# Optimization experiments

Measured on AMD Instinct MI355X. Metric: run time of the kernel, lower is better.

Reference implementation:

```python
import jax, jax.numpy as jnp
import numpy as np

N_HEAD = 16
HEAD_DIM = 64

def setup_inputs() -> dict:
    key = jax.random.key(0)
    k1, k2, k3 = jax.random.split(key, 3)
    B, S, D = 4, 2048, 1024
    x = jax.random.normal(k1, (B, S, D), dtype=jnp.float32)
    mask = jnp.tril(jnp.ones((S, S), dtype=bool))[None, None]  # (1,1,S,S) causal
    w_attn = jax.random.normal(k2, (D, 3 * D), dtype=jnp.float32) * (1.0 / np.sqrt(D))
    b_attn = jnp.zeros((3 * D,), dtype=jnp.float32)
    w_proj = jax.random.normal(k3, (D, D), dtype=jnp.float32) * (1.0 / np.sqrt(D))
    b_proj = jnp.zeros((D,), dtype=jnp.float32)
    return {"x": x, "mask": mask, "w_attn": w_attn, "b_attn": b_attn,
            "w_proj": w_proj, "b_proj": b_proj}

def reference(x, mask, w_attn, b_attn, w_proj, b_proj):
    B, S, D = x.shape
    H, hd = N_HEAD, HEAD_DIM
    qkv = x @ w_attn + b_attn                      # (B,S,3D)
    q, k, v = jnp.split(qkv, 3, axis=-1)
    q = q.reshape(B, S, H, hd).transpose(0, 2, 1, 3)  # (B,H,S,hd)
    k = k.reshape(B, S, H, hd).transpose(0, 2, 1, 3)
    v = v.reshape(B, S, H, hd).transpose(0, 2, 1, 3)
    scores = jnp.einsum('bhqd,bhkd->bhqk', q, k) / jnp.sqrt(jnp.float32(hd))
    scores = jnp.where(mask, scores, jnp.float32(-1e10))
    weights = jax.nn.softmax(scores, axis=-1)      # dropout is identity (deterministic=True)
    attn = jnp.einsum('bhqk,bhkd->bhqd', weights, v)
    attn = attn.transpose(0, 2, 1, 3).reshape(B, S, D)
    return attn @ w_proj + b_proj
```

## Files before the change

### kernel.cpp

```cpp
#include <hip/hip_runtime.h>
#include <hip/hip_bf16.h>
#include <stdint.h>


typedef uint16_t u16;
typedef __bf16 bf16x8 __attribute__((ext_vector_type(8)));
typedef __bf16 bf16x4 __attribute__((ext_vector_type(4)));
typedef short s16x4 __attribute__((ext_vector_type(4)));
typedef float f32x4 __attribute__((ext_vector_type(4)));

#define S_LEN 2048
#define DMODEL 1024
#define NHEAD 16
#define HDIM 64
#define MTOT 8192
#define NQKV 3072

__device__ __forceinline__ u16 f2bf(float f) {
    union { float f; uint32_t u; } v; v.f = f;
    uint32_t u = v.u;
    return (u16)((u + 0x7fffu + ((u >> 16) & 1u)) >> 16);
}

__device__ __forceinline__ s16x4 bits4(bf16x4 v) {
    union { bf16x4 b; s16x4 s; } u; u.b = v; return u.s;
}

__device__ __forceinline__ f32x4 mfma16(bf16x4 a, bf16x4 b, f32x4 c) {
    return __builtin_amdgcn_mfma_f32_16x16x16bf16_1k(bits4(a), bits4(b), c, 0, 0, 0);
}

__device__ __forceinline__ void async_load16(const void* g, void* l) {
    __builtin_amdgcn_global_load_lds(
        (__attribute__((address_space(1))) void*)g,
        (__attribute__((address_space(3))) void*)l,
        16, 0, 0);
}

__global__ void convert_x_kernel(const float4* __restrict__ in, ushort4* __restrict__ out, int n4) {
    int i = blockIdx.x * 256 + threadIdx.x;
    if (i < n4) {
        float4 f = in[i];
        ushort4 o;
        o.x = f2bf(f.x); o.y = f2bf(f.y); o.z = f2bf(f.z); o.w = f2bf(f.w);
        out[i] = o;
    }
}

__global__ void transpose_bf16_kernel(const float* __restrict__ in, u16* __restrict__ out, int R, int C) {
    __shared__ float tile[64][65];
    int r0 = blockIdx.y * 64, c0 = blockIdx.x * 64;
    #pragma unroll
    for (int i = 0; i < 16; ++i) {
        int idx = threadIdx.x + i * 256;
        int r = idx >> 6, c = idx & 63;
        tile[r][c] = in[(size_t)(r0 + r) * C + c0 + c];
    }
    __syncthreads();
    #pragma unroll
    for (int i = 0; i < 16; ++i) {
        int idx = threadIdx.x + i * 256;
        int c = idx >> 6, r = idx & 63;
        out[(size_t)(c0 + c) * R + r0 + r] = f2bf(tile[r][c]);
    }
}

__global__ void transpose_v_kernel(const u16* __restrict__ qkv, u16* __restrict__ vt) {
    __shared__ u16 tile[64 * 66];
    const int tid = threadIdx.x;
    const int stile = blockIdx.x, bh = blockIdx.y;
    const int b = bh >> 4, h = bh & 15;
    const u16* src = qkv + ((size_t)b * S_LEN + stile * 64) * NQKV + 2 * DMODEL + h * HDIM;
    #pragma unroll
    for (int it = 0; it < 2; ++it) {
        int item = it * 256 + tid;
        int s = item >> 3, d0 = (item & 7) * 8;
        bf16x8 v = *(const bf16x8*)(src + (size_t)s * NQKV + d0);
        const u16* vu = (const u16*)&v;
        #pragma unroll
        for (int j = 0; j < 8; ++j) tile[(d0 + j) * 66 + s] = vu[j];
    }
    __syncthreads();
    #pragma unroll
    for (int it = 0; it < 2; ++it) {
        int item = it * 256 + tid;
        int d = item >> 3, s0 = (item & 7) * 8;
        union { u16 u[8]; uint4 v; } pk;
        #pragma unroll
        for (int j = 0; j < 8; ++j) pk.u[j] = tile[d * 66 + s0 + j];
        *(uint4*)(vt + ((size_t)bh * 64 + d) * S_LEN + stile * 64 + s0) = pk.v;
    }
}

template<bool OUT_BF16>
__global__ __launch_bounds__(256, 3) void gemm_bt(
    const u16* __restrict__ A, const u16* __restrict__ Bt,
    const float* __restrict__ bias, void* __restrict__ C,
    int M, int N, int K)
{
    __shared__ __attribute__((aligned(16))) u16 As[128 * 32];
    __shared__ __attribute__((aligned(16))) u16 Bs[128 * 32];
    const int tid = threadIdx.x;
    const int wave = tid >> 6, lane = tid & 63;
    const int l15 = lane & 15, q4 = lane >> 4;
    const int wm = wave >> 1, wn = wave & 1;

    const int gx = gridDim.x, gy = gridDim.y;
    int bid = (int)blockIdx.y * gx + (int)blockIdx.x;
    const int PANEL = 8;
    int panel = bid / (PANEL * gy);
    int within = bid - panel * (PANEL * gy);
    int mb = panel * PANEL + (within % PANEL);
    int nb = within / PANEL;
    const int m0 = mb * 128, n0 = nb * 128;

    f32x4 acc[4][4] = {};

    const int srow = lane >> 2;
    const int scol = (lane & 3) * 8;

    for (int k0 = 0; k0 < K; k0 += 32) {
        #pragma unroll
        for (int q = 0; q < 2; ++q) {
            int r = wave * 32 + q * 16 + srow;
            async_load16(A  + (size_t)(m0 + r) * K + k0 + scol, As + (wave * 32 + q * 16) * 32);
            async_load16(Bt + (size_t)(n0 + r) * K + k0 + scol, Bs + (wave * 32 + q * 16) * 32);
        }
        __syncthreads();

        bf16x8 af[4], bfr[4];
        #pragma unroll
        for (int t = 0; t < 4; ++t) {
            af[t]  = *(const bf16x8*)(As + (wm * 64 + t * 16 + l15) * 32 + q4 * 8);
            bfr[t] = *(const bf16x8*)(Bs + (wn * 64 + t * 16 + l15) * 32 + q4 * 8);
        }
        #pragma unroll
        for (int tm = 0; tm < 4; ++tm)
            #pragma unroll
            for (int tn = 0; tn < 4; ++tn)
                acc[tm][tn] = __builtin_amdgcn_mfma_f32_16x16x32_bf16(af[tm], bfr[tn], acc[tm][tn], 0, 0, 0);
        __syncthreads();
    }

    #pragma unroll
    for (int tm = 0; tm < 4; ++tm) {
        int row = m0 + wm * 64 + tm * 16 + q4 * 4;
        #pragma unroll
        for (int tn = 0; tn < 4; ++tn) {
            int col = n0 + wn * 64 + tn * 16 + l15;
            float bv = bias[col];
            #pragma unroll
            for (int r2 = 0; r2 < 4; ++r2) {
                float v = acc[tm][tn][r2] + bv;
                if (OUT_BF16) ((u16*)C)[(size_t)(row + r2) * N + col] = f2bf(v);
                else          ((float*)C)[(size_t)(row + r2) * N + col] = v;
            }
        }
    }
}

__device__ __forceinline__ void stage_tiles(
    const u16* __restrict__ qkv, const u16* __restrict__ vt,
    size_t base, int bh, int h, int w, int srow8, int schunk,
    int kt, u16* __restrict__ KsB, u16* __restrict__ VsB)
{
    #pragma unroll
    for (int q = 0; q < 2; ++q) {
        int rloc = w * 16 + q * 8 + srow8;
        int sc = ((schunk ^ (rloc & 7)) * 8);
        async_load16(qkv + (base + (size_t)kt * 64 + rloc) * (size_t)NQKV + DMODEL + h * HDIM + sc,
                     KsB + (w * 16 + q * 8) * 64);
        async_load16(vt + ((size_t)bh * 64 + rloc) * S_LEN + kt * 64 + sc,
                     VsB + (w * 16 + q * 8) * 64);
    }
}

__device__ __forceinline__ void attn_pass(
    int qt, const u16* __restrict__ qkv, const u16* __restrict__ vt,
    __bf16* __restrict__ outb, u16 (*Ks)[64 * 64], u16 (*Vs)[64 * 64],
    int w, int lane, int bh, int h, size_t base)
{
    const int l15 = lane & 15, q4 = lane >> 4;
    const int srow8 = lane >> 3, schunk = lane & 7;

    const float QSCALE = 0.125f * 1.44269504f;
    bf16x8 qf[2][2];
    #pragma unroll
    for (int mh = 0; mh < 2; ++mh) {
        int qrow = qt * 128 + mh * 64 + w * 16 + l15;
        #pragma unroll
        for (int kc = 0; kc < 2; ++kc) {
            bf16x8 raw = *(const bf16x8*)(qkv + (base + qrow) * (size_t)NQKV + h * HDIM + kc * 32 + q4 * 8);
            bf16x8 sc;
            #pragma unroll
            for (int j = 0; j < 8; ++j) sc[j] = (__bf16)((float)raw[j] * QSCALE);
            qf[mh][kc] = sc;
        }
    }

    bf16x4 ones4;
    #pragma unroll
    for (int j = 0; j < 4; ++j) ones4[j] = (__bf16)1.0f;

    f32x4 o0[4] = {}, o1[4] = {};
    f32x4 la0 = {}, la1 = {};

    const int ktlast = 2 * qt + 1;

    __syncthreads();
    stage_tiles(qkv, vt, base, bh, h, w, srow8, schunk, 0, Ks[0], Vs[0]);
    if (ktlast >= 1)
        stage_tiles(qkv, vt, base, bh, h, w, srow8, schunk, 1, Ks[1], Vs[1]);

    for (int kt = 0; kt <= 2 * qt; ++kt) {
        const int buf = kt % 3;
        __syncthreads();
        int pf = kt + 2;
        if (pf <= ktlast)
            stage_tiles(qkv, vt, base, bh, h, w, srow8, schunk, pf, Ks[pf % 3], Vs[pf % 3]);

        f32x4 st0[4] = {}, st1[4] = {};
        #pragma unroll
        for (int nt = 0; nt < 4; ++nt) {
            int n = nt * 16 + l15;
            #pragma unroll
            for (int kc = 0; kc < 2; ++kc) {
                int ch = (((kc * 4 + q4) ^ (n & 7)) * 8);
                bf16x8 kf = *(const bf16x8*)(&Ks[buf][n * 64 + ch]);
                st0[nt] = __builtin_amdgcn_mfma_f32_16x16x32_bf16(kf, qf[0][kc], st0[nt], 0, 0, 0);
                st1[nt] = __builtin_amdgcn_mfma_f32_16x16x32_bf16(kf, qf[1][kc], st1[nt], 0, 0, 0);
            }
        }

        if (kt == 2 * qt) {
            #pragma unroll
            for (int nt = 0; nt < 4; ++nt)
                #pragma unroll
                for (int r = 0; r < 4; ++r) {
                    int keyl = nt * 16 + q4 * 4 + r;
                    if (keyl > w * 16 + l15) st0[nt][r] = -1e30f;
                }
        }

        bf16x4 pb0[4], pb1[4];
        #pragma unroll
        for (int nt = 0; nt < 4; ++nt)
            #pragma unroll
            for (int r = 0; r < 4; ++r) {
                pb0[nt][r] = (__bf16)__builtin_amdgcn_exp2f(st0[nt][r]);
                pb1[nt][r] = (__bf16)__builtin_amdgcn_exp2f(st1[nt][r]);
            }

        #pragma unroll
        for (int nt = 0; nt < 4; ++nt) {
            #pragma unroll
            for (int mt = 0; mt < 4; ++mt) {
                int row = mt * 16 + l15;
                int ch = (nt * 2 + (q4 >> 1)) ^ (row & 7);
                bf16x4 vf = *(const bf16x4*)(&Vs[buf][row * 64 + ch * 8 + (q4 & 1) * 4]);
                o0[mt] = mfma16(vf, pb0[nt], o0[mt]);
                o1[mt] = mfma16(vf, pb1[nt], o1[mt]);
            }
            la0 = mfma16(ones4, pb0[nt], la0);
            la1 = mfma16(ones4, pb1[nt], la1);
        }
    }

    {
        const int buf = ktlast % 3;
        __syncthreads();

        f32x4 st1[4] = {};
        #pragma unroll
        for (int nt = 0; nt < 4; ++nt) {
            int n = nt * 16 + l15;
            #pragma unroll
            for (int kc = 0; kc < 2; ++kc) {
                int ch = (((kc * 4 + q4) ^ (n & 7)) * 8);
                bf16x8 kf = *(const bf16x8*)(&Ks[buf][n * 64 + ch]);
                st1[nt] = __builtin_amdgcn_mfma_f32_16x16x32_bf16(kf, qf[1][kc], st1[nt], 0, 0, 0);
            }
        }
        bf16x4 pb1[4];
        #pragma unroll
        for (int nt = 0; nt < 4; ++nt)
            #pragma unroll
            for (int r = 0; r < 4; ++r) {
                int keyl = nt * 16 + q4 * 4 + r;
                float s = (keyl > w * 16 + l15) ? -1e30f : st1[nt][r];
                pb1[nt][r] = (__bf16)__builtin_amdgcn_exp2f(s);
            }
        #pragma unroll
        for (int nt = 0; nt < 4; ++nt) {
            #pragma unroll
            for (int mt = 0; mt < 4; ++mt) {
                int row = mt * 16 + l15;
                int ch = (nt * 2 + (q4 >> 1)) ^ (row & 7);
                bf16x4 vf = *(const bf16x4*)(&Vs[buf][row * 64 + ch * 8 + (q4 & 1) * 4]);
                o1[mt] = mfma16(vf, pb1[nt], o1[mt]);
            }
            la1 = mfma16(ones4, pb1[nt], la1);
        }
    }

    float inv0 = 1.0f / la0[0], inv1 = 1.0f / la1[0];
    int row0 = qt * 128 + w * 16 + l15;
    int row1 = row0 + 64;
    #pragma unroll
    for (int mt = 0; mt < 4; ++mt) {
        union { __bf16 b[4]; ushort4 v; } p0, p1;
        #pragma unroll
        for (int r = 0; r < 4; ++r) {
            p0.b[r] = (__bf16)(o0[mt][r] * inv0);
            p1.b[r] = (__bf16)(o1[mt][r] * inv1);
        }
        int col = h * HDIM + mt * 16 + q4 * 4;
        *(ushort4*)(&outb[(base + row0) * (size_t)DMODEL + col]) = p0.v;
        *(ushort4*)(&outb[(base + row1) * (size_t)DMODEL + col]) = p1.v;
    }
}

__global__ __launch_bounds__(256, 3) void attn_kernel(
    const u16* __restrict__ qkv, const u16* __restrict__ vt, u16* __restrict__ out)
{
    __shared__ __attribute__((aligned(16))) u16 Ks[3][64 * 64];
    __shared__ __attribute__((aligned(16))) u16 Vs[3][64 * 64];

    const int tid = threadIdx.x;
    const int w = tid >> 6, lane = tid & 63;
    const int bh = blockIdx.y;
    const int b = bh >> 4, h = bh & 15;
    const size_t base = (size_t)b * S_LEN;
    const int NT = (int)gridDim.x * 2;

    attn_pass(NT - 1 - (int)blockIdx.x, qkv, vt, (__bf16*)out, Ks, Vs, w, lane, bh, h, base);
    attn_pass((int)blockIdx.x,          qkv, vt, (__bf16*)out, Ks, Vs, w, lane, bh, h, base);
}

extern "C" void kernel_launch(void* const* d_in, const int* in_sizes, int n_in,
                              void* d_out, int out_size, void* d_ws, size_t ws_size,
                              hipStream_t stream) {
    const float* x      = (const float*)d_in[0];
    const float* w_attn = (const float*)d_in[2];
    const float* b_attn = (const float*)d_in[3];
    const float* w_proj = (const float*)d_in[4];
    const float* b_proj = (const float*)d_in[5];

    u16* xb   = (u16*)d_ws;
    u16* wat  = xb  + (size_t)MTOT * DMODEL;
    u16* wpt  = wat + (size_t)NQKV * DMODEL;
    u16* qkv  = wpt + (size_t)DMODEL * DMODEL;
    u16* attn = qkv + (size_t)MTOT * NQKV;
    u16* vt   = xb;

    convert_x_kernel<<<(MTOT * DMODEL / 4 + 255) / 256, 256, 0, stream>>>(
        (const float4*)x, (ushort4*)xb, MTOT * DMODEL / 4);
    transpose_bf16_kernel<<<dim3(NQKV / 64, DMODEL / 64), 256, 0, stream>>>(w_attn, wat, DMODEL, NQKV);
    transpose_bf16_kernel<<<dim3(DMODEL / 64, DMODEL / 64), 256, 0, stream>>>(w_proj, wpt, DMODEL, DMODEL);

    gemm_bt<true><<<dim3(MTOT / 128, NQKV / 128), 256, 0, stream>>>(
        xb, wat, b_attn, (void*)qkv, MTOT, NQKV, DMODEL);

    transpose_v_kernel<<<dim3(S_LEN / 64, 4 * NHEAD), 256, 0, stream>>>(qkv, vt);

    attn_kernel<<<dim3(S_LEN / 256, 4 * NHEAD), 256, 0, stream>>>(qkv, vt, attn);

    gemm_bt<false><<<dim3(MTOT / 128, DMODEL / 128), 256, 0, stream>>>(
        attn, wpt, b_proj, d_out, MTOT, DMODEL, DMODEL);
}
```

Before: 270.8 us.

## Replace GEMM with 256x128-tile, 512-thread double-buffered pipelined kernel

Swaps the 128x128 single-stage GEMM for a 256x128 tile kernel with 8 waves and K=64 steps. Global-to-LDS loads are double-buffered and overlapped with MFMA work using explicit vmcnt waits and barriers. LDS chunks are XOR-swizzled to avoid bank conflicts, workgroups are remapped for L2 locality, and setprio is raised around the MFMA blocks. The aim is to hide memory latency and cut per-K-step sync overhead in both projections. The cost is 96KB of LDS per block and fragile hand-written waitcnt ordering.

```diff
diff --git a/kernel.cpp b/kernel.cpp
--- a/kernel.cpp
+++ b/kernel.cpp
@@ -93,67 +93,143 @@
 }
 
 template<bool OUT_BF16>
-__global__ __launch_bounds__(256, 3) void gemm_bt(
+__global__ __launch_bounds__(512, 2) void gemm256(
     const u16* __restrict__ A, const u16* __restrict__ Bt,
     const float* __restrict__ bias, void* __restrict__ C,
     int M, int N, int K)
 {
-    __shared__ __attribute__((aligned(16))) u16 As[128 * 32];
-    __shared__ __attribute__((aligned(16))) u16 Bs[128 * 32];
+    __shared__ __attribute__((aligned(16))) u16 sm[49152];
     const int tid = threadIdx.x;
     const int wave = tid >> 6, lane = tid & 63;
     const int l15 = lane & 15, q4 = lane >> 4;
-    const int wm = wave >> 1, wn = wave & 1;
-
-    const int gx = gridDim.x, gy = gridDim.y;
-    int bid = (int)blockIdx.y * gx + (int)blockIdx.x;
-    const int PANEL = 8;
-    int panel = bid / (PANEL * gy);
-    int within = bid - panel * (PANEL * gy);
-    int mb = panel * PANEL + (within % PANEL);
-    int nb = within / PANEL;
-    const int m0 = mb * 128, n0 = nb * 128;
+    const int wm = wave & 3, wn = wave >> 2;
+
+    const int nwg = (int)gridDim.x;
+    const int bid = (int)blockIdx.x;
+    const int wg = (bid & 7) * (nwg >> 3) + (bid >> 3);
+    const int MB = M >> 8;
+    const int mb = wg & (MB - 1);
+    const int nb = wg / MB;
+    const int m0 = mb << 8, n0 = nb << 7;
+
+    const u16* Ag = A + (size_t)m0 * K;
+    const u16* Bg = Bt + (size_t)n0 * K;
+
+    const int srow = tid >> 3;
+    const size_t goff0 = (size_t)srow * K + (size_t)(((tid & 7) ^ (srow & 7)) * 8);
+    const size_t goff1 = goff0 + (size_t)64 * K;
+    const int ldso = tid * 8;
+
+    const int ck0 = (q4 ^ (l15 & 7)) * 8;
+    const int ck1 = ((4 + q4) ^ (l15 & 7)) * 8;
+    const int ra0 = (wm * 32 + l15) * 64;
+    const int ra1 = ra0 + 16 * 64;
+    const int rb0 = (wn * 64 + l15) * 64;
 
     f32x4 acc[4][4] = {};
-
-    const int srow = lane >> 2;
-    const int scol = (lane & 3) * 8;
-
-    for (int k0 = 0; k0 < K; k0 += 32) {
-        #pragma unroll
-        for (int q = 0; q < 2; ++q) {
-            int r = wave * 32 + q * 16 + srow;
-            async_load16(A  + (size_t)(m0 + r) * K + k0 + scol, As + (wave * 32 + q * 16) * 32);
-            async_load16(Bt + (size_t)(n0 + r) * K + k0 + scol, Bs + (wave * 32 + q * 16) * 32);
-        }
-        __syncthreads();
-
-        bf16x8 af[4], bfr[4];
-        #pragma unroll
-        for (int t = 0; t < 4; ++t) {
-            af[t]  = *(const bf16x8*)(As + (wm * 64 + t * 16 + l15) * 32 + q4 * 8);
-            bfr[t] = *(const bf16x8*)(Bs + (wn * 64 + t * 16 + l15) * 32 + q4 * 8);
-        }
-        #pragma unroll
-        for (int tm = 0; tm < 4; ++tm)
-            #pragma unroll
-            for (int tn = 0; tn < 4; ++tn)
-                acc[tm][tn] = __builtin_amdgcn_mfma_f32_16x16x32_bf16(af[tm], bfr[tn], acc[tm][tn], 0, 0, 0);
-        __syncthreads();
-    }
-
-    #pragma unroll
-    for (int tm = 0; tm < 4; ++tm) {
-        int row = m0 + wm * 64 + tm * 16 + q4 * 4;
-        #pragma unroll
-        for (int tn = 0; tn < 4; ++tn) {
-            int col = n0 + wn * 64 + tn * 16 + l15;
-            float bv = bias[col];
-            #pragma unroll
-            for (int r2 = 0; r2 < 4; ++r2) {
-                float v = acc[tm][tn][r2] + bv;
-                if (OUT_BF16) ((u16*)C)[(size_t)(row + r2) * N + col] = f2bf(v);
-                else          ((float*)C)[(size_t)(row + r2) * N + col] = v;
+    const int T = K >> 6;
+
+    u16* const As = sm;
+    u16* const Bs = sm + 32768;
+
+    {
+        async_load16(Ag + goff0, As + ldso);
+        async_load16(Ag + goff1, As + ldso + 4096);
+        async_load16(Bg + goff0, Bs + ldso);
+        async_load16(Bg + goff1, Bs + ldso + 4096);
+        async_load16(Ag + (size_t)128 * K + goff0, As + 8192 + ldso);
+        async_load16(Ag + (size_t)128 * K + goff1, As + 8192 + ldso + 4096);
+        if (T > 1) {
+            async_load16(Ag + 64 + goff0, As + 2 * 8192 + ldso);
+            async_load16(Ag + 64 + goff1, As + 2 * 8192 + ldso + 4096);
+            async_load16(Bg + 64 + goff0, Bs + 8192 + ldso);
+            async_load16(Bg + 64 + goff1, Bs + 8192 + ldso + 4096);
+            asm volatile("s_waitcnt vmcnt(4)" ::: "memory");
+        } else {
+            asm volatile("s_waitcnt vmcnt(0)" ::: "memory");
+        }
+        asm volatile("s_barrier" ::: "memory");
+    }
+
+    for (int t = 0; t < T; ++t) {
+        const int par = t & 1;
+        const u16* As0 = As + par * 2 * 8192;
+        const u16* As1 = As0 + 8192;
+        const u16* Bsl = Bs + par * 8192;
+
+        bf16x8 bfr[4][2], afr[2][2];
+        #pragma unroll
+        for (int nf = 0; nf < 4; ++nf) {
+            bfr[nf][0] = *(const bf16x8*)(Bsl + rb0 + nf * (16 * 64) + ck0);
+            bfr[nf][1] = *(const bf16x8*)(Bsl + rb0 + nf * (16 * 64) + ck1);
+        }
+        afr[0][0] = *(const bf16x8*)(As0 + ra0 + ck0);
+        afr[0][1] = *(const bf16x8*)(As0 + ra0 + ck1);
+        afr[1][0] = *(const bf16x8*)(As0 + ra1 + ck0);
+        afr[1][1] = *(const bf16x8*)(As0 + ra1 + ck1);
+        if (t + 1 < T) {
+            const u16* g = Ag + (size_t)128 * K + (size_t)(t + 1) * 64;
+            u16* l = As + ((par ^ 1) * 2 + 1) * 8192;
+            async_load16(g + goff0, l + ldso);
+            async_load16(g + goff1, l + ldso + 4096);
+        }
+        asm volatile("s_barrier" ::: "memory");
+        __builtin_amdgcn_s_setprio(1);
+        #pragma unroll
+        for (int m = 0; m < 2; ++m)
+            #pragma unroll
+            for (int nf = 0; nf < 4; ++nf)
+                #pragma unroll
+                for (int kk = 0; kk < 2; ++kk)
+                    acc[m][nf] = __builtin_amdgcn_mfma_f32_16x16x32_bf16(
+                        afr[m][kk], bfr[nf][kk], acc[m][nf], 0, 0, 0);
+        __builtin_amdgcn_s_setprio(0);
+        asm volatile("s_barrier" ::: "memory");
+
+        afr[0][0] = *(const bf16x8*)(As1 + ra0 + ck0);
+        afr[0][1] = *(const bf16x8*)(As1 + ra0 + ck1);
+        afr[1][0] = *(const bf16x8*)(As1 + ra1 + ck0);
+        afr[1][1] = *(const bf16x8*)(As1 + ra1 + ck1);
+        if (t + 2 < T) {
+            const u16* ga = Ag + (size_t)(t + 2) * 64;
+            const u16* gb = Bg + (size_t)(t + 2) * 64;
+            u16* la = As + par * 2 * 8192;
+            u16* lb = Bs + par * 8192;
+            async_load16(ga + goff0, la + ldso);
+            async_load16(ga + goff1, la + ldso + 4096);
+            async_load16(gb + goff0, lb + ldso);
+            async_load16(gb + goff1, lb + ldso + 4096);
+        }
+        asm volatile("s_barrier" ::: "memory");
+        __builtin_amdgcn_s_setprio(1);
+        #pragma unroll
+        for (int m = 0; m < 2; ++m)
+            #pragma unroll
+            for (int nf = 0; nf < 4; ++nf)
+                #pragma unroll
+                for (int kk = 0; kk < 2; ++kk)
+                    acc[2 + m][nf] = __builtin_amdgcn_mfma_f32_16x16x32_bf16(
+                        afr[m][kk], bfr[nf][kk], acc[2 + m][nf], 0, 0, 0);
+        __builtin_amdgcn_s_setprio(0);
+        if (t + 1 < T) {
+            if (t + 2 < T) asm volatile("s_waitcnt vmcnt(4)" ::: "memory");
+            else           asm volatile("s_waitcnt vmcnt(0)" ::: "memory");
+            asm volatile("s_barrier" ::: "memory");
+        }
+    }
+
+    #pragma unroll
+    for (int mf = 0; mf < 4; ++mf) {
+        const int row = m0 + (mf >> 1) * 128 + wm * 32 + (mf & 1) * 16 + q4 * 4;
+        #pragma unroll
+        for (int nf = 0; nf < 4; ++nf) {
+            const int col = n0 + wn * 64 + nf * 16 + l15;
+            const float bv = bias[col];
+            #pragma unroll
+            for (int r = 0; r < 4; ++r) {
+                float v = acc[mf][nf][r] + bv;
+                if (OUT_BF16) ((u16*)C)[(size_t)(row + r) * N + col] = f2bf(v);
+                else          ((float*)C)[(size_t)(row + r) * N + col] = v;
             }
         }
     }
@@ -358,13 +434,13 @@
     transpose_bf16_kernel<<<dim3(NQKV / 64, DMODEL / 64), 256, 0, stream>>>(w_attn, wat, DMODEL, NQKV);
     transpose_bf16_kernel<<<dim3(DMODEL / 64, DMODEL / 64), 256, 0, stream>>>(w_proj, wpt, DMODEL, DMODEL);
 
-    gemm_bt<true><<<dim3(MTOT / 128, NQKV / 128), 256, 0, stream>>>(
+    gemm256<true><<<dim3((MTOT / 256) * (NQKV / 128)), 512, 0, stream>>>(
         xb, wat, b_attn, (void*)qkv, MTOT, NQKV, DMODEL);
 
     transpose_v_kernel<<<dim3(S_LEN / 64, 4 * NHEAD), 256, 0, stream>>>(qkv, vt);
 
     attn_kernel<<<dim3(S_LEN / 256, 4 * NHEAD), 256, 0, stream>>>(qkv, vt, attn);
 
-    gemm_bt<false><<<dim3(MTOT / 128, DMODEL / 128), 256, 0, stream>>>(
+    gemm256<false><<<dim3((MTOT / 256) * (DMODEL / 128)), 512, 0, stream>>>(
         attn, wpt, b_proj, d_out, MTOT, DMODEL, DMODEL);
 }
```

Result: slower. 285.0 us (+5.3%).
